# Optimization experiments

Hardware: AMD Instinct MI355X
Metric: run time of the kernel (lower is better)

Reference implementation:

```python
import jax, jax.numpy as jnp
import numpy as np

B, D, C = 4096, 768, 80
PRIV = np.arange(0, 20)        # privileged label indices
NONPRIV = np.arange(20, 80)    # non-privileged label indices
EPS = 1e-8
BETA = 1.0
EPSILON = 0.1
DIMS = [768, 256, 64, 16, 4, 1]


def setup_inputs() -> dict:
    key = jax.random.key(0)
    ks = jax.random.split(key, 12)
    inp = {
        "hidden": jax.random.normal(ks[0], (B, D), dtype=jnp.float32),
        "labels": jax.random.randint(ks[1], (B, C), 0, 2, dtype=jnp.int32),
    }
    ki = 2
    for wpref, bpref in (("W", "b"), ("rW", "rb")):
        for i in range(5):
            din, dout = DIMS[i], DIMS[i + 1]
            inp[f"{wpref}{i+1}"] = (jax.random.normal(ks[ki], (C, din, dout), dtype=jnp.float32)
                                     * (1.0 / np.sqrt(din)))
            inp[f"{bpref}{i+1}"] = jnp.zeros((C, dout), dtype=jnp.float32)
            ki += 1
    return inp


def _scores(hidden, Ws, bs):
    # c independent MLP heads applied to the same hidden state, batched over c.
    x = jnp.einsum('bd,cdh->bch', hidden, Ws[0]) + bs[0]  # (b, c, 256)
    for W, b in zip(Ws[1:], bs[1:]):
        x = jnp.einsum('bch,cho->bco', jax.nn.relu(x), W) + b
    return jax.nn.sigmoid(x[..., 0])  # (b, c)


def _bce(p, y):
    p = jnp.clip(p, EPS, 1.0 - EPS)
    return -(y * jnp.log(p) + (1.0 - y) * jnp.log1p(-p))


def _losses(scores, ref_scores, labels):
    ref_scores = jax.lax.stop_gradient(ref_scores)  # ref head is frozen
    # --- privileged pairwise margin loss (vectorized masked form) ---
    log_term = jnp.log(scores / (ref_scores + EPS) + EPS)  # (b, c)
    ps = scores[:, PRIV]                                   # (b, P)
    pos = labels[:, PRIV] == 1                             # (b, P)
    neg = labels == 0                                      # (b, c)
    # confusing negative k for positive privileged l: y_k==0 and s_k >= s_l
    conf = pos[:, :, None] & neg[:, None, :] & (scores[:, None, :] >= ps[:, :, None])
    h_w = log_term[:, PRIV][:, :, None] - log_term[:, None, :]   # (b, P, c)
    pair_loss = -jax.nn.log_sigmoid(BETA * h_w)
    n_pairs = conf.sum()
    total = jnp.where(conf, pair_loss, 0.0).sum()
    loss_priv = jnp.where(n_pairs > 0, total / jnp.maximum(n_pairs, 1), 0.0)
    # --- non-privileged hinged BCE ---
    y = labels[:, NONPRIV].astype(jnp.float32)
    loss_cur = _bce(scores[:, NONPRIV], y)
    loss_ref = jax.lax.stop_gradient(_bce(ref_scores[:, NONPRIV], y))
    loss_nonpriv = jnp.mean(jax.nn.relu(loss_cur - loss_ref - EPSILON))
    return jnp.stack([loss_priv, loss_nonpriv])


def reference(hidden, labels, W1, b1, W2, b2, W3, b3, W4, b4, W5, b5,
              rW1, rb1, rW2, rb2, rW3, rb3, rW4, rb4, rW5, rb5):
    scores = _scores(hidden, (W1, W2, W3, W4, W5), (b1, b2, b3, b4, b5))
    ref_scores = _scores(hidden, (rW1, rW2, rW3, rW4, rW5), (rb1, rb2, rb3, rb4, rb5))
    return _losses(scores, ref_scores, labels)
```

## Files before the change

kernel.cpp:

```cpp
#include <hip/hip_runtime.h>
#include <math.h>

typedef __attribute__((ext_vector_type(8))) short short8;
typedef __attribute__((ext_vector_type(4))) float f32x4;

#define Bn   4096
#define Dn   768
#define Cn   80
#define H1   256
#define H2   64
#define H3   16
#define H4   4

__device__ inline ushort f2bf(float f) {
    union { float f; unsigned u; } v; v.f = f;
    unsigned r = v.u + 0x7fffu + ((v.u >> 16) & 1u);
    return (ushort)(r >> 16);
}
__device__ inline unsigned pack2(float a, float b) {
    return (unsigned)f2bf(a) | ((unsigned)f2bf(b) << 16);
}
__device__ inline void load_lds16(const void* g, void* l) {
    __builtin_amdgcn_global_load_lds(
        (const __attribute__((address_space(1))) void*)g,
        (__attribute__((address_space(3))) void*)l, 16, 0, 0);
}

#define FENCE() asm volatile("" ::: "memory")
#define BAR() do { FENCE(); __builtin_amdgcn_sched_barrier(0); \
                   __builtin_amdgcn_s_barrier(); \
                   __builtin_amdgcn_sched_barrier(0); FENCE(); } while (0)
#define VMCNT4() do { asm volatile("s_waitcnt vmcnt(4)" ::: "memory"); \
                      __builtin_amdgcn_sched_barrier(0); } while (0)
#define VMCNT0() do { asm volatile("s_waitcnt vmcnt(0)" ::: "memory"); \
                      __builtin_amdgcn_sched_barrier(0); } while (0)

__global__ __launch_bounds__(256)
void convert_hidden(const float* __restrict__ hidden, ushort* __restrict__ hbs)
{
    const int t = threadIdx.x;
    const int kt = blockIdx.x;
    const int bt = blockIdx.y;
    char* out = (char*)(hbs + ((size_t)bt * 12 + kt) * 4096);
    #pragma unroll
    for (int ch = 0; ch < 2; ++ch) {
        const int o = (ch * 256 + t) * 16;
        const int row = o >> 7;
        const int slot = (o >> 4) & 7;
        const int ss = slot ^ (row & 7);
        const float* src = hidden + (size_t)(bt * 64 + row) * Dn + kt * 64 + ss * 8;
        const float4 f0 = ((const float4*)src)[0];
        const float4 f1 = ((const float4*)src)[1];
        uint4 w;
        w.x = pack2(f0.x, f0.y); w.y = pack2(f0.z, f0.w);
        w.z = pack2(f1.x, f1.y); w.w = pack2(f1.z, f1.w);
        *(uint4*)(out + o) = w;
    }
}

__global__ __launch_bounds__(256)
void convert_w1(const float* __restrict__ W, const float* __restrict__ rW,
                ushort* __restrict__ dst)
{
    __shared__ float l[32 * H1];
    const int t   = threadIdx.x;
    const int kt2 = blockIdx.x;
    const int c   = blockIdx.y;
    const int set = blockIdx.z;
    const float* src = (set ? rW : W) + ((size_t)c * Dn + kt2 * 32) * H1;
    #pragma unroll
    for (int i = 0; i < 8; ++i)
        ((float4*)l)[i * 256 + t] = ((const float4*)src)[i * 256 + t];
    __syncthreads();
    char* out = (char*)dst + (((size_t)set * Cn + c) * 24 + kt2) * 16384;
    #pragma unroll
    for (int rd = 0; rd < 4; ++rd) {
        const int o = (rd * 256 + t) * 16;
        const int n = o >> 6;
        const int s = (o >> 4) & 3;
        const int kk0 = (s ^ (n & 3)) * 8;
        uint4 w;
        w.x = pack2(l[(kk0 + 0) * H1 + n], l[(kk0 + 1) * H1 + n]);
        w.y = pack2(l[(kk0 + 2) * H1 + n], l[(kk0 + 3) * H1 + n]);
        w.z = pack2(l[(kk0 + 4) * H1 + n], l[(kk0 + 5) * H1 + n]);
        w.w = pack2(l[(kk0 + 6) * H1 + n], l[(kk0 + 7) * H1 + n]);
        *(uint4*)(out + o) = w;
    }
}

__global__ __launch_bounds__(256)
void convert_w23(const float* __restrict__ W2, const float* __restrict__ rW2,
                 const float* __restrict__ W3, const float* __restrict__ rW3,
                 ushort* __restrict__ dstW2, ushort* __restrict__ dstW3)
{
    __shared__ float l[64 * H2];
    const int t   = threadIdx.x;
    const int bx  = blockIdx.x;
    const int c   = blockIdx.y;
    const int set = blockIdx.z;

    if (bx < 4) {
        const float* src = (set ? rW2 : W2) + ((size_t)c * H1 + bx * 64) * H2;
        #pragma unroll
        for (int i = 0; i < 4; ++i)
            ((float4*)l)[i * 256 + t] = ((const float4*)src)[i * 256 + t];
        __syncthreads();
        char* out = (char*)dstW2 + (((size_t)set * Cn + c) * 4 + bx) * 8192;
        #pragma unroll
        for (int rd = 0; rd < 2; ++rd) {
            const int idx = rd * 256 + t;
            const int n = idx >> 3;
            const int s = idx & 7;
            const int o = n * 128 + ((s << 4) ^ ((n & 7) << 4));
            const int kk0 = s * 8;
            uint4 w;
            w.x = pack2(l[(kk0 + 0) * H2 + n], l[(kk0 + 1) * H2 + n]);
            w.y = pack2(l[(kk0 + 2) * H2 + n], l[(kk0 + 3) * H2 + n]);
            w.z = pack2(l[(kk0 + 4) * H2 + n], l[(kk0 + 5) * H2 + n]);
            w.w = pack2(l[(kk0 + 6) * H2 + n], l[(kk0 + 7) * H2 + n]);
            *(uint4*)(out + o) = w;
        }
    } else if (t < 128) {
        const float* src = (set ? rW3 : W3) + (size_t)c * (H2 * H3);
        char* out = (char*)dstW3 + ((size_t)set * Cn + c) * 2048;
        const int o = t * 16;
        const int n = o >> 7;
        const int slot = (o >> 4) & 7;
        const int kk0 = (slot ^ (n & 7)) * 8;
        uint4 w;
        w.x = pack2(src[(kk0 + 0) * H3 + n], src[(kk0 + 1) * H3 + n]);
        w.y = pack2(src[(kk0 + 2) * H3 + n], src[(kk0 + 3) * H3 + n]);
        w.z = pack2(src[(kk0 + 4) * H3 + n], src[(kk0 + 5) * H3 + n]);
        w.w = pack2(src[(kk0 + 6) * H3 + n], src[(kk0 + 7) * H3 + n]);
        *(uint4*)(out + o) = w;
    }
}


__device__ __forceinline__ void stage_a(char* lds, const char* hbs_b, int p, int h,
                                        int kt, int bt0, int t) {
    const char* g = hbs_b + ((size_t)((bt0 + h * 2) * 12 + kt)) * 8192 + t * 16;
    char* l = lds + p * 32768 + h * 16384 + t * 16;
    load_lds16(g,         l);
    load_lds16(g + 98304, l + 8192);
}
__device__ __forceinline__ void stage_b(char* lds, const char* w1b, int p, int kh,
                                        int kt, int t) {
    const char* g = w1b + ((size_t)(kt * 2 + kh)) * 16384 + t * 16;
    char* l = lds + 65536 + p * 32768 + kh * 16384 + t * 16;
    load_lds16(g,        l);
    load_lds16(g + 8192, l + 8192);
}

template<int KS, int MH>
__device__ __forceinline__ void phase_reads(const char* lds, int p, int wr, int wc,
                                            int lrow, int lk, short8 breg[4], short8 areg[4]) {
    if (MH == 0) {
        #pragma unroll
        for (int nt = 0; nt < 4; ++nt) {
            const int col = wc * 64 + nt * 16 + lrow;
            breg[nt] = *(const short8*)(lds + 65536 + p * 32768 + KS * 16384
                          + col * 64 + ((2 * lk) ^ ((col & 3) << 4)));
        }
    }
    #pragma unroll
    for (int m4 = 0; m4 < 4; ++m4) {
        const int mt = MH * 4 + m4;
        const int ir = (mt & 3) * 16 + lrow;
        const int koff = KS * 64 + lk * 2;
        areg[m4] = *(const short8*)(lds + p * 32768 + (wr * 2 + (mt >> 2)) * 8192
                      + ir * 128 + (koff ^ ((ir & 7) << 4)));
    }
}

template<int MH>
__device__ __forceinline__ void phase_mfma(const short8 breg[4], const short8 areg[4],
                                           f32x4 acc[8][4]) {
    __builtin_amdgcn_s_setprio(1);
    #pragma unroll
    for (int m4 = 0; m4 < 4; ++m4)
        #pragma unroll
        for (int nt = 0; nt < 4; ++nt)
            acc[MH * 4 + m4][nt] = __builtin_amdgcn_mfma_f32_16x16x32_bf16(
                breg[nt], areg[m4], acc[MH * 4 + m4][nt], 0, 0, 0);
    __builtin_amdgcn_s_setprio(0);
}

__global__ __launch_bounds__(512, 2)
void scores_mfma_256(const ushort* __restrict__ hbs, const ushort* __restrict__ W1ts,
                     const ushort* __restrict__ W2ts, const ushort* __restrict__ W3ts,
                     const float* __restrict__ b1, const float* __restrict__ rb1,
                     const float* __restrict__ b2, const float* __restrict__ rb2,
                     const float* __restrict__ b3, const float* __restrict__ rb3,
                     const float* __restrict__ W4, const float* __restrict__ rW4,
                     const float* __restrict__ b4, const float* __restrict__ rb4,
                     const float* __restrict__ W5, const float* __restrict__ rW5,
                     const float* __restrict__ b5, const float* __restrict__ rb5,
                     float* __restrict__ scores)
{
    __shared__ uint4 smv[131072 / 16];
    char* lds = (char*)smv;

    const int t = threadIdx.x;
    const int wid = t >> 6, lane = t & 63;
    const int lrow = lane & 15;
    const int lkg  = lane >> 4;
    const int lk   = lkg * 8;
    const int wr = wid >> 2, wc = wid & 3;

    const int cpx = 2560 >> 3;
    const int wg  = (blockIdx.x & 7) * cpx + (blockIdx.x >> 3);
    const int set = wg / 1280;
    const int rem = wg % 1280;
    const int c   = rem / 16;
    const int bt0 = (rem % 16) * 4;

    const float* pb1 = set ? rb1 : b1;
    const float* pb2 = set ? rb2 : b2;
    const float* pb3 = set ? rb3 : b3;
    const float* pW4 = set ? rW4 : W4;  const float* pb4 = set ? rb4 : b4;
    const float* pW5 = set ? rW5 : W5;  const float* pb5 = set ? rb5 : b5;

    const char* hbs_b = (const char*)hbs;
    const char* w1b   = (const char*)W1ts + (size_t)(set * Cn + c) * 393216;

    f32x4 acc[8][4];
    #pragma unroll
    for (int i = 0; i < 8; ++i)
        #pragma unroll
        for (int j = 0; j < 4; ++j)
            acc[i][j] = (f32x4){0.f, 0.f, 0.f, 0.f};

    stage_a(lds, hbs_b, 0, 0, 0, bt0, t);
    stage_a(lds, hbs_b, 0, 1, 0, bt0, t);
    stage_b(lds, w1b, 0, 0, 0, t);
    stage_b(lds, w1b, 0, 1, 0, t);
    stage_b(lds, w1b, 1, 0, 1, t);
    stage_b(lds, w1b, 1, 1, 1, t);
    VMCNT4();
    BAR();

    short8 breg[4], areg[4];
    for (int j = 0; j < 12; ++j) {
        const int p  = j & 1;
        const int ja = (j + 1) % 12;
        const int jb = (j + 2) % 12;
        phase_reads<0, 0>(lds, p, wr, wc, lrow, lk, breg, areg);
        stage_a(lds, hbs_b, p ^ 1, 0, ja, bt0, t);
        BAR(); phase_mfma<0>(breg, areg, acc); BAR();
        phase_reads<0, 1>(lds, p, wr, wc, lrow, lk, breg, areg);
        stage_a(lds, hbs_b, p ^ 1, 1, ja, bt0, t);
        BAR(); phase_mfma<1>(breg, areg, acc); BAR();
        phase_reads<1, 0>(lds, p, wr, wc, lrow, lk, breg, areg);
        stage_b(lds, w1b, p, 0, jb, t);
        BAR(); phase_mfma<0>(breg, areg, acc); BAR();
        phase_reads<1, 1>(lds, p, wr, wc, lrow, lk, breg, areg);
        stage_b(lds, w1b, p, 1, jb, t);
        VMCNT4();
        BAR(); phase_mfma<1>(breg, areg, acc); BAR();
    }
    VMCNT0();
    BAR();

    {
        float4 bias1[4];
        #pragma unroll
        for (int nt = 0; nt < 4; ++nt)
            bias1[nt] = *(const float4*)&pb1[(size_t)c * H1 + wc * 64 + nt * 16 + lkg * 4];
        #pragma unroll
        for (int mt = 0; mt < 8; ++mt) {
            const int row = wr * 128 + mt * 16 + lrow;
            const int swz = (row & 7) << 4;
            #pragma unroll
            for (int nt = 0; nt < 4; ++nt) {
                const float* bb = (const float*)&bias1[nt];
                uint2 w;
                w.x = pack2(fmaxf(acc[mt][nt][0] + bb[0], 0.f),
                            fmaxf(acc[mt][nt][1] + bb[1], 0.f));
                w.y = pack2(fmaxf(acc[mt][nt][2] + bb[2], 0.f),
                            fmaxf(acc[mt][nt][3] + bb[3], 0.f));
                const int off = row * 512 + ((wc * 128 + nt * 32 + lkg * 8) ^ swz);
                *(uint2*)(lds + off) = w;
            }
        }
    }
    BAR();

    f32x4 acc2[2][4];
    #pragma unroll
    for (int i = 0; i < 2; ++i)
        #pragma unroll
        for (int j = 0; j < 4; ++j)
            acc2[i][j] = (f32x4){0.f, 0.f, 0.f, 0.f};
    {
        const char* w2b = (const char*)W2ts + (size_t)(set * Cn + c) * 32768;
        #pragma unroll
        for (int ksz = 0; ksz < 8; ++ksz) {
            short8 b2r[4], a2[2];
            const int kk2 = (ksz & 1) * 32 + lk;
            #pragma unroll
            for (int nt = 0; nt < 4; ++nt) {
                const int col = nt * 16 + lrow;
                b2r[nt] = *(const short8*)(w2b + (ksz >> 1) * 8192
                             + ((col * 128 + 2 * kk2) ^ ((col & 7) << 4)));
            }
            const int k = ksz * 32 + lk;
            #pragma unroll
            for (int m2 = 0; m2 < 2; ++m2) {
                const int row = wid * 32 + m2 * 16 + lrow;
                a2[m2] = *(const short8*)(lds + ((row * 512 + 2 * k) ^ ((row & 7) << 4)));
            }
            #pragma unroll
            for (int m2 = 0; m2 < 2; ++m2)
                #pragma unroll
                for (int nt = 0; nt < 4; ++nt)
                    acc2[m2][nt] = __builtin_amdgcn_mfma_f32_16x16x32_bf16(
                        b2r[nt], a2[m2], acc2[m2][nt], 0, 0, 0);
        }
    }
    BAR();

    {
        float4 bias2[4];
        #pragma unroll
        for (int nt = 0; nt < 4; ++nt)
            bias2[nt] = *(const float4*)&pb2[(size_t)c * H2 + nt * 16 + lkg * 4];
        #pragma unroll
        for (int m2 = 0; m2 < 2; ++m2) {
            const int row = wid * 32 + m2 * 16 + lrow;
            const int swz = (row & 7) << 4;
            #pragma unroll
            for (int nt = 0; nt < 4; ++nt) {
                const float* bb = (const float*)&bias2[nt];
                uint2 w;
                w.x = pack2(fmaxf(acc2[m2][nt][0] + bb[0], 0.f),
                            fmaxf(acc2[m2][nt][1] + bb[1], 0.f));
                w.y = pack2(fmaxf(acc2[m2][nt][2] + bb[2], 0.f),
                            fmaxf(acc2[m2][nt][3] + bb[3], 0.f));
                const int off = row * 128 + ((nt * 32 + lkg * 8) ^ swz);
                *(uint2*)(lds + off) = w;
            }
        }
    }
    BAR();

    {
        const char* w3t = (const char*)W3ts + (size_t)(set * Cn + c) * 2048;
        short8 w3f[2];
        #pragma unroll
        for (int ks = 0; ks < 2; ++ks)
            w3f[ks] = *(const short8*)(w3t + lrow * 128
                         + ((2 * (ks * 32 + lk)) ^ ((lrow & 7) << 4)));
        f32x4 acc3[2];
        #pragma unroll
        for (int m2 = 0; m2 < 2; ++m2) acc3[m2] = (f32x4){0.f, 0.f, 0.f, 0.f};
        #pragma unroll
        for (int m2 = 0; m2 < 2; ++m2)
            #pragma unroll
            for (int ks = 0; ks < 2; ++ks) {
                const int row = wid * 32 + m2 * 16 + lrow;
                const short8 xf = *(const short8*)(lds + row * 128
                                     + ((2 * (ks * 32 + lk)) ^ ((row & 7) << 4)));
                acc3[m2] = __builtin_amdgcn_mfma_f32_16x16x32_bf16(
                    w3f[ks], xf, acc3[m2], 0, 0, 0);
            }

        const float4 b3v = *(const float4*)&pb3[(size_t)c * H3 + lkg * 4];
        const float* w4c = pW4 + (size_t)c * (H3 * H4);
        float4 w4r[4];
        #pragma unroll
        for (int r = 0; r < 4; ++r)
            w4r[r] = *(const float4*)&w4c[(lkg * 4 + r) * H4];
        const float4 b4v = *(const float4*)&pb4[(size_t)c * H4];
        const float4 w5v = *(const float4*)&pW5[(size_t)c * H4];
        const float bb5 = pb5[c];

        #pragma unroll
        for (int m2 = 0; m2 < 2; ++m2) {
            float p4[4] = {0.f, 0.f, 0.f, 0.f};
            #pragma unroll
            for (int r = 0; r < 4; ++r) {
                const float x3 = fmaxf(acc3[m2][r] + ((const float*)&b3v)[r], 0.f);
                const float* wr4 = (const float*)&w4r[r];
                #pragma unroll
                for (int o = 0; o < 4; ++o)
                    p4[o] = fmaf(x3, wr4[o], p4[o]);
            }
            #pragma unroll
            for (int o = 0; o < 4; ++o) {
                p4[o] += __shfl_xor(p4[o], 16, 64);
                p4[o] += __shfl_xor(p4[o], 32, 64);
            }
            float x5 = bb5;
            #pragma unroll
            for (int o = 0; o < 4; ++o)
                x5 = fmaf(fmaxf(p4[o] + ((const float*)&b4v)[o], 0.f),
                          ((const float*)&w5v)[o], x5);
            const float sc = 1.f / (1.f + expf(-x5));
            if (lkg == 0)
                scores[((size_t)set * Bn + bt0 * 64 + wid * 32 + m2 * 16 + lrow) * Cn + c] = sc;
        }
    }
}

__device__ inline float bce_f(float p, float y) {
    p = fminf(fmaxf(p, 1e-8f), 1.0f - 1e-8f);
    return -(y * logf(p) + (1.f - y) * log1pf(-p));
}

__global__ __launch_bounds__(128)
void loss_kernel(const float* __restrict__ scores, const int* __restrict__ labels,
                 float* __restrict__ pair_sum, float* __restrict__ np_sum,
                 int* __restrict__ pair_cnt)
{
    __shared__ float ss[Cn], lt[Cn];
    __shared__ int lab[Cn];
    __shared__ float redf[128], redn[128];
    __shared__ int redi[128];

    const int b = blockIdx.x, t = threadIdx.x;
    float np_local = 0.f, ps_local = 0.f;
    int pc_local = 0;

    if (t < Cn) {
        const float s  = scores[(size_t)b * Cn + t];
        const float sr = scores[(size_t)Bn * Cn + (size_t)b * Cn + t];
        const int l = labels[(size_t)b * Cn + t];
        ss[t] = s; lab[t] = l;
        lt[t] = logf(s / (sr + 1e-8f) + 1e-8f);
        if (t >= 20) {
            const float y = (float)l;
            np_local = fmaxf(bce_f(s, y) - bce_f(sr, y) - 0.1f, 0.f);
        }
    }
    __syncthreads();
    if (t < Cn && lab[t] == 0) {
        const float sj = ss[t], ltj = lt[t];
        #pragma unroll
        for (int i = 0; i < 20; ++i) {
            if (lab[i] == 1 && sj >= ss[i]) {
                const float z = -(lt[i] - ltj);
                ps_local += fmaxf(z, 0.f) + log1pf(expf(-fabsf(z)));
                pc_local++;
            }
        }
    }
    redf[t] = ps_local; redn[t] = np_local; redi[t] = pc_local;
    __syncthreads();
    for (int s = 64; s > 0; s >>= 1) {
        if (t < s) { redf[t] += redf[t + s]; redn[t] += redn[t + s]; redi[t] += redi[t + s]; }
        __syncthreads();
    }
    if (t == 0) { pair_sum[b] = redf[0]; np_sum[b] = redn[0]; pair_cnt[b] = redi[0]; }
}

__global__ __launch_bounds__(1024)
void final_kernel(const float* __restrict__ pair_sum, const int* __restrict__ pair_cnt,
                  const float* __restrict__ np_sum, float* __restrict__ out)
{
    __shared__ float r1[1024], r2[1024];
    __shared__ int ri[1024];
    const int t = threadIdx.x;
    float s1 = 0.f, s2 = 0.f; int c1 = 0;
    for (int i = t; i < Bn; i += 1024) { s1 += pair_sum[i]; c1 += pair_cnt[i]; s2 += np_sum[i]; }
    r1[t] = s1; r2[t] = s2; ri[t] = c1;
    __syncthreads();
    for (int s = 512; s > 0; s >>= 1) {
        if (t < s) { r1[t] += r1[t + s]; r2[t] += r2[t + s]; ri[t] += ri[t + s]; }
        __syncthreads();
    }
    if (t == 0) {
        const int n = ri[0];
        out[0] = (n > 0) ? (r1[0] / (float)(n > 1 ? n : 1)) : 0.f;
        out[1] = r2[0] / (float)(Bn * 60);
    }
}

static inline size_t alup(size_t x) { return (x + 4095) & ~(size_t)4095; }

extern "C" void kernel_launch(void* const* d_in, const int* in_sizes, int n_in,
                              void* d_out, int out_size, void* d_ws, size_t ws_size,
                              hipStream_t stream)
{
    const float* hidden = (const float*)d_in[0];
    const int*   labels = (const int*)d_in[1];
    const float* W1 = (const float*)d_in[2];   const float* b1 = (const float*)d_in[3];
    const float* W2 = (const float*)d_in[4];   const float* b2 = (const float*)d_in[5];
    const float* W3 = (const float*)d_in[6];   const float* b3 = (const float*)d_in[7];
    const float* W4 = (const float*)d_in[8];   const float* b4 = (const float*)d_in[9];
    const float* W5 = (const float*)d_in[10];  const float* b5 = (const float*)d_in[11];
    const float* rW1 = (const float*)d_in[12]; const float* rb1 = (const float*)d_in[13];
    const float* rW2 = (const float*)d_in[14]; const float* rb2 = (const float*)d_in[15];
    const float* rW3 = (const float*)d_in[16]; const float* rb3 = (const float*)d_in[17];
    const float* rW4 = (const float*)d_in[18]; const float* rb4 = (const float*)d_in[19];
    const float* rW5 = (const float*)d_in[20]; const float* rb5 = (const float*)d_in[21];

    char* ws = (char*)d_ws;
    const size_t off_scores = 0;
    const size_t sz_scores  = (size_t)2 * Bn * Cn * 4;
    const size_t off_pair   = alup(off_scores + sz_scores);
    const size_t sz_pair    = (size_t)3 * Bn * 4;
    const size_t off_hbs    = alup(off_pair + sz_pair);
    const size_t sz_hbs     = (size_t)Bn * Dn * 2;
    const size_t off_w1t    = alup(off_hbs + sz_hbs);
    const size_t sz_w1t     = (size_t)2 * Cn * 24 * 16384;
    const size_t off_w2t    = alup(off_w1t + sz_w1t);
    const size_t sz_w2t     = (size_t)2 * Cn * 4 * 8192;
    const size_t off_w3t    = alup(off_w2t + sz_w2t);

    float* scoresb  = (float*)(ws + off_scores);
    float* pair_sum = (float*)(ws + off_pair);
    float* np_sum   = pair_sum + Bn;
    int*   pair_cnt = (int*)(np_sum + Bn);
    float* out      = (float*)d_out;

    ushort* hbs  = (ushort*)(ws + off_hbs);
    ushort* W1ts = (ushort*)(ws + off_w1t);
    ushort* W2ts = (ushort*)(ws + off_w2t);
    ushort* W3ts = (ushort*)(ws + off_w3t);

    convert_hidden<<<dim3(12, Bn / 64), 256, 0, stream>>>(hidden, hbs);
    convert_w1<<<dim3(24, Cn, 2), 256, 0, stream>>>(W1, rW1, W1ts);
    convert_w23<<<dim3(5, Cn, 2), 256, 0, stream>>>(W2, rW2, W3, rW3, W2ts, W3ts);

    scores_mfma_256<<<2560, 512, 0, stream>>>(hbs, W1ts, W2ts, W3ts,
        b1, rb1, b2, rb2, b3, rb3, W4, rW4, b4, rb4, W5, rW5, b5, rb5,
        scoresb);
    loss_kernel<<<Bn, 128, 0, stream>>>(scoresb, labels, pair_sum, np_sum, pair_cnt);
    final_kernel<<<1, 1024, 0, stream>>>(pair_sum, pair_cnt, np_sum, out);
}
```

Before: 353.6 us.

## Shrink fused MLP tile to 128 rows with triple-buffered K=32 pipeline

Reworks the main scores kernel from 256-row tiles to 128-row tiles, doubling the grid and cutting LDS from 128KB to 72KB so four 512-thread blocks may fit per CU. The K loop changes from a double-buffered 64-wide step split into four phases to a triple-buffered 32-wide step with one MFMA burst per iteration. The hidden-state conversion layout and swizzle change to match. This raises occupancy and simplifies the pipeline, at the cost of loading each W1 slice twice as often (half the reuse per load) and more barriers per unit of work.

```diff
diff --git a/kernel.cpp b/kernel.cpp
--- a/kernel.cpp
+++ b/kernel.cpp
@@ -30,7 +30,7 @@
 #define BAR() do { FENCE(); __builtin_amdgcn_sched_barrier(0); \
                    __builtin_amdgcn_s_barrier(); \
                    __builtin_amdgcn_sched_barrier(0); FENCE(); } while (0)
-#define VMCNT4() do { asm volatile("s_waitcnt vmcnt(4)" ::: "memory"); \
+#define VMCNT3() do { asm volatile("s_waitcnt vmcnt(3)" ::: "memory"); \
                       __builtin_amdgcn_sched_barrier(0); } while (0)
 #define VMCNT0() do { asm volatile("s_waitcnt vmcnt(0)" ::: "memory"); \
                       __builtin_amdgcn_sched_barrier(0); } while (0)
@@ -41,14 +41,14 @@
     const int t = threadIdx.x;
     const int kt = blockIdx.x;
     const int bt = blockIdx.y;
-    char* out = (char*)(hbs + ((size_t)bt * 12 + kt) * 4096);
+    char* out = (char*)hbs + ((size_t)bt * 24 + kt) * 8192;
     #pragma unroll
     for (int ch = 0; ch < 2; ++ch) {
         const int o = (ch * 256 + t) * 16;
-        const int row = o >> 7;
-        const int slot = (o >> 4) & 7;
-        const int ss = slot ^ (row & 7);
-        const float* src = hidden + (size_t)(bt * 64 + row) * Dn + kt * 64 + ss * 8;
+        const int r = o >> 6;
+        const int s = (o >> 4) & 3;
+        const int k0 = (s ^ (r & 3)) * 8;
+        const float* src = hidden + (size_t)(bt * 128 + r) * Dn + kt * 32 + k0;
         const float4 f0 = ((const float4*)src)[0];
         const float4 f1 = ((const float4*)src)[1];
         uint4 w;
@@ -137,57 +137,18 @@
 }
 
 
-__device__ __forceinline__ void stage_a(char* lds, const char* hbs_b, int p, int h,
-                                        int kt, int bt0, int t) {
-    const char* g = hbs_b + ((size_t)((bt0 + h * 2) * 12 + kt)) * 8192 + t * 16;
-    char* l = lds + p * 32768 + h * 16384 + t * 16;
-    load_lds16(g,         l);
-    load_lds16(g + 98304, l + 8192);
-}
-__device__ __forceinline__ void stage_b(char* lds, const char* w1b, int p, int kh,
-                                        int kt, int t) {
-    const char* g = w1b + ((size_t)(kt * 2 + kh)) * 16384 + t * 16;
-    char* l = lds + 65536 + p * 32768 + kh * 16384 + t * 16;
+__device__ __forceinline__ void stageA(char* lds, const char* hb, int slot, int kt, int t) {
+    load_lds16(hb + (size_t)kt * 8192 + t * 16, lds + slot * 8192 + t * 16);
+}
+__device__ __forceinline__ void stageB(char* lds, const char* w1b, int slot, int kt, int t) {
+    const char* g = w1b + (size_t)kt * 16384 + t * 16;
+    char* l = lds + 24576 + slot * 16384 + t * 16;
     load_lds16(g,        l);
     load_lds16(g + 8192, l + 8192);
 }
 
-template<int KS, int MH>
-__device__ __forceinline__ void phase_reads(const char* lds, int p, int wr, int wc,
-                                            int lrow, int lk, short8 breg[4], short8 areg[4]) {
-    if (MH == 0) {
-        #pragma unroll
-        for (int nt = 0; nt < 4; ++nt) {
-            const int col = wc * 64 + nt * 16 + lrow;
-            breg[nt] = *(const short8*)(lds + 65536 + p * 32768 + KS * 16384
-                          + col * 64 + ((2 * lk) ^ ((col & 3) << 4)));
-        }
-    }
-    #pragma unroll
-    for (int m4 = 0; m4 < 4; ++m4) {
-        const int mt = MH * 4 + m4;
-        const int ir = (mt & 3) * 16 + lrow;
-        const int koff = KS * 64 + lk * 2;
-        areg[m4] = *(const short8*)(lds + p * 32768 + (wr * 2 + (mt >> 2)) * 8192
-                      + ir * 128 + (koff ^ ((ir & 7) << 4)));
-    }
-}
-
-template<int MH>
-__device__ __forceinline__ void phase_mfma(const short8 breg[4], const short8 areg[4],
-                                           f32x4 acc[8][4]) {
-    __builtin_amdgcn_s_setprio(1);
-    #pragma unroll
-    for (int m4 = 0; m4 < 4; ++m4)
-        #pragma unroll
-        for (int nt = 0; nt < 4; ++nt)
-            acc[MH * 4 + m4][nt] = __builtin_amdgcn_mfma_f32_16x16x32_bf16(
-                breg[nt], areg[m4], acc[MH * 4 + m4][nt], 0, 0, 0);
-    __builtin_amdgcn_s_setprio(0);
-}
-
-__global__ __launch_bounds__(512, 2)
-void scores_mfma_256(const ushort* __restrict__ hbs, const ushort* __restrict__ W1ts,
+__global__ __launch_bounds__(512, 4)
+void scores_mfma_128(const ushort* __restrict__ hbs, const ushort* __restrict__ W1ts,
                      const ushort* __restrict__ W2ts, const ushort* __restrict__ W3ts,
                      const float* __restrict__ b1, const float* __restrict__ rb1,
                      const float* __restrict__ b2, const float* __restrict__ rb2,
@@ -198,7 +159,7 @@
                      const float* __restrict__ b5, const float* __restrict__ rb5,
                      float* __restrict__ scores)
 {
-    __shared__ uint4 smv[131072 / 16];
+    __shared__ uint4 smv[73728 / 16];
     char* lds = (char*)smv;
 
     const int t = threadIdx.x;
@@ -208,12 +169,12 @@
     const int lk   = lkg * 8;
     const int wr = wid >> 2, wc = wid & 3;
 
-    const int cpx = 2560 >> 3;
+    const int cpx = 5120 >> 3;
     const int wg  = (blockIdx.x & 7) * cpx + (blockIdx.x >> 3);
-    const int set = wg / 1280;
-    const int rem = wg % 1280;
-    const int c   = rem / 16;
-    const int bt0 = (rem % 16) * 4;
+    const int set = wg / 2560;
+    const int rem = wg % 2560;
+    const int c   = rem / 32;
+    const int bt  = rem % 32;
 
     const float* pb1 = set ? rb1 : b1;
     const float* pb2 = set ? rb2 : b2;
@@ -221,43 +182,56 @@
     const float* pW4 = set ? rW4 : W4;  const float* pb4 = set ? rb4 : b4;
     const float* pW5 = set ? rW5 : W5;  const float* pb5 = set ? rb5 : b5;
 
-    const char* hbs_b = (const char*)hbs;
-    const char* w1b   = (const char*)W1ts + (size_t)(set * Cn + c) * 393216;
-
-    f32x4 acc[8][4];
+    const char* hb  = (const char*)hbs + (size_t)bt * 196608;
+    const char* w1b = (const char*)W1ts + (size_t)(set * Cn + c) * 393216;
+
+    f32x4 acc[4][4];
     #pragma unroll
-    for (int i = 0; i < 8; ++i)
+    for (int i = 0; i < 4; ++i)
         #pragma unroll
         for (int j = 0; j < 4; ++j)
             acc[i][j] = (f32x4){0.f, 0.f, 0.f, 0.f};
 
-    stage_a(lds, hbs_b, 0, 0, 0, bt0, t);
-    stage_a(lds, hbs_b, 0, 1, 0, bt0, t);
-    stage_b(lds, w1b, 0, 0, 0, t);
-    stage_b(lds, w1b, 0, 1, 0, t);
-    stage_b(lds, w1b, 1, 0, 1, t);
-    stage_b(lds, w1b, 1, 1, 1, t);
-    VMCNT4();
+    stageA(lds, hb, 0, 0, t);  stageB(lds, w1b, 0, 0, t);
+    stageA(lds, hb, 1, 1, t);  stageB(lds, w1b, 1, 1, t);
+    VMCNT3();
     BAR();
 
-    short8 breg[4], areg[4];
-    for (int j = 0; j < 12; ++j) {
-        const int p  = j & 1;
-        const int ja = (j + 1) % 12;
-        const int jb = (j + 2) % 12;
-        phase_reads<0, 0>(lds, p, wr, wc, lrow, lk, breg, areg);
-        stage_a(lds, hbs_b, p ^ 1, 0, ja, bt0, t);
-        BAR(); phase_mfma<0>(breg, areg, acc); BAR();
-        phase_reads<0, 1>(lds, p, wr, wc, lrow, lk, breg, areg);
-        stage_a(lds, hbs_b, p ^ 1, 1, ja, bt0, t);
-        BAR(); phase_mfma<1>(breg, areg, acc); BAR();
-        phase_reads<1, 0>(lds, p, wr, wc, lrow, lk, breg, areg);
-        stage_b(lds, w1b, p, 0, jb, t);
-        BAR(); phase_mfma<0>(breg, areg, acc); BAR();
-        phase_reads<1, 1>(lds, p, wr, wc, lrow, lk, breg, areg);
-        stage_b(lds, w1b, p, 1, jb, t);
-        VMCNT4();
-        BAR(); phase_mfma<1>(breg, areg, acc); BAR();
+    #pragma unroll 3
+    for (int j = 0; j < 24; ++j) {
+        const int rs = j % 3;
+        short8 breg[4], areg[4];
+        {
+            const char* bb = lds + 24576 + rs * 16384;
+            const char* ab = lds + rs * 8192;
+            #pragma unroll
+            for (int nt = 0; nt < 4; ++nt) {
+                const int col = wc * 64 + nt * 16 + lrow;
+                breg[nt] = *(const short8*)(bb + col * 64 + ((2 * lk) ^ ((col & 3) << 4)));
+            }
+            #pragma unroll
+            for (int mt = 0; mt < 4; ++mt) {
+                const int row = wr * 64 + mt * 16 + lrow;
+                areg[mt] = *(const short8*)(ab + row * 64 + ((2 * lk) ^ ((row & 3) << 4)));
+            }
+        }
+        {
+            const int ws = (j + 2) % 3;
+            int ka = j + 2; if (ka >= 24) ka -= 24;
+            stageA(lds, hb, ws, ka, t);
+            stageB(lds, w1b, ws, ka, t);
+        }
+        VMCNT3();
+        BAR();
+        __builtin_amdgcn_s_setprio(1);
+        #pragma unroll
+        for (int mt = 0; mt < 4; ++mt)
+            #pragma unroll
+            for (int nt = 0; nt < 4; ++nt)
+                acc[mt][nt] = __builtin_amdgcn_mfma_f32_16x16x32_bf16(
+                    breg[nt], areg[mt], acc[mt][nt], 0, 0, 0);
+        __builtin_amdgcn_s_setprio(0);
+        BAR();
     }
     VMCNT0();
     BAR();
@@ -268,8 +242,8 @@
         for (int nt = 0; nt < 4; ++nt)
             bias1[nt] = *(const float4*)&pb1[(size_t)c * H1 + wc * 64 + nt * 16 + lkg * 4];
         #pragma unroll
-        for (int mt = 0; mt < 8; ++mt) {
-            const int row = wr * 128 + mt * 16 + lrow;
+        for (int mt = 0; mt < 4; ++mt) {
+            const int row = wr * 64 + mt * 16 + lrow;
             const int swz = (row & 7) << 4;
             #pragma unroll
             for (int nt = 0; nt < 4; ++nt) {
@@ -286,17 +260,16 @@
     }
     BAR();
 
-    f32x4 acc2[2][4];
+    f32x4 acc2[4];
     #pragma unroll
-    for (int i = 0; i < 2; ++i)
-        #pragma unroll
-        for (int j = 0; j < 4; ++j)
-            acc2[i][j] = (f32x4){0.f, 0.f, 0.f, 0.f};
+    for (int j = 0; j < 4; ++j) acc2[j] = (f32x4){0.f, 0.f, 0.f, 0.f};
     {
         const char* w2b = (const char*)W2ts + (size_t)(set * Cn + c) * 32768;
+        const int row = wid * 16 + lrow;
+        const int swzr = (row & 7) << 4;
         #pragma unroll
         for (int ksz = 0; ksz < 8; ++ksz) {
-            short8 b2r[4], a2[2];
+            short8 b2r[4];
             const int kk2 = (ksz & 1) * 32 + lk;
             #pragma unroll
             for (int nt = 0; nt < 4; ++nt) {
@@ -305,41 +278,29 @@
                              + ((col * 128 + 2 * kk2) ^ ((col & 7) << 4)));
             }
             const int k = ksz * 32 + lk;
-            #pragma unroll
-            for (int m2 = 0; m2 < 2; ++m2) {
-                const int row = wid * 32 + m2 * 16 + lrow;
-                a2[m2] = *(const short8*)(lds + ((row * 512 + 2 * k) ^ ((row & 7) << 4)));
-            }
-            #pragma unroll
-            for (int m2 = 0; m2 < 2; ++m2)
-                #pragma unroll
-                for (int nt = 0; nt < 4; ++nt)
-                    acc2[m2][nt] = __builtin_amdgcn_mfma_f32_16x16x32_bf16(
-                        b2r[nt], a2[m2], acc2[m2][nt], 0, 0, 0);
+            const short8 a2 = *(const short8*)(lds + ((row * 512 + 2 * k) ^ swzr));
+            #pragma unroll
+            for (int nt = 0; nt < 4; ++nt)
+                acc2[nt] = __builtin_amdgcn_mfma_f32_16x16x32_bf16(
+                    b2r[nt], a2, acc2[nt], 0, 0, 0);
         }
     }
     BAR();
 
     {
-        float4 bias2[4];
-        #pragma unroll
-        for (int nt = 0; nt < 4; ++nt)
-            bias2[nt] = *(const float4*)&pb2[(size_t)c * H2 + nt * 16 + lkg * 4];
-        #pragma unroll
-        for (int m2 = 0; m2 < 2; ++m2) {
-            const int row = wid * 32 + m2 * 16 + lrow;
-            const int swz = (row & 7) << 4;
-            #pragma unroll
-            for (int nt = 0; nt < 4; ++nt) {
-                const float* bb = (const float*)&bias2[nt];
-                uint2 w;
-                w.x = pack2(fmaxf(acc2[m2][nt][0] + bb[0], 0.f),
-                            fmaxf(acc2[m2][nt][1] + bb[1], 0.f));
-                w.y = pack2(fmaxf(acc2[m2][nt][2] + bb[2], 0.f),
-                            fmaxf(acc2[m2][nt][3] + bb[3], 0.f));
-                const int off = row * 128 + ((nt * 32 + lkg * 8) ^ swz);
-                *(uint2*)(lds + off) = w;
-            }
+        const int row = wid * 16 + lrow;
+        const int swz = (row & 7) << 4;
+        #pragma unroll
+        for (int nt = 0; nt < 4; ++nt) {
+            const float4 bv = *(const float4*)&pb2[(size_t)c * H2 + nt * 16 + lkg * 4];
+            const float* bb = (const float*)&bv;
+            uint2 w;
+            w.x = pack2(fmaxf(acc2[nt][0] + bb[0], 0.f),
+                        fmaxf(acc2[nt][1] + bb[1], 0.f));
+            w.y = pack2(fmaxf(acc2[nt][2] + bb[2], 0.f),
+                        fmaxf(acc2[nt][3] + bb[3], 0.f));
+            const int off = row * 128 + ((nt * 32 + lkg * 8) ^ swz);
+            *(uint2*)(lds + off) = w;
         }
     }
     BAR();
@@ -351,19 +312,14 @@
         for (int ks = 0; ks < 2; ++ks)
             w3f[ks] = *(const short8*)(w3t + lrow * 128
                          + ((2 * (ks * 32 + lk)) ^ ((lrow & 7) << 4)));
-        f32x4 acc3[2];
-        #pragma unroll
-        for (int m2 = 0; m2 < 2; ++m2) acc3[m2] = (f32x4){0.f, 0.f, 0.f, 0.f};
-        #pragma unroll
-        for (int m2 = 0; m2 < 2; ++m2)
-            #pragma unroll
-            for (int ks = 0; ks < 2; ++ks) {
-                const int row = wid * 32 + m2 * 16 + lrow;
-                const short8 xf = *(const short8*)(lds + row * 128
-                                     + ((2 * (ks * 32 + lk)) ^ ((row & 7) << 4)));
-                acc3[m2] = __builtin_amdgcn_mfma_f32_16x16x32_bf16(
-                    w3f[ks], xf, acc3[m2], 0, 0, 0);
-            }
+        f32x4 acc3 = (f32x4){0.f, 0.f, 0.f, 0.f};
+        const int row = wid * 16 + lrow;
+        #pragma unroll
+        for (int ks = 0; ks < 2; ++ks) {
+            const short8 xf = *(const short8*)(lds + row * 128
+                                 + ((2 * (ks * 32 + lk)) ^ ((row & 7) << 4)));
+            acc3 = __builtin_amdgcn_mfma_f32_16x16x32_bf16(w3f[ks], xf, acc3, 0, 0, 0);
+        }
 
         const float4 b3v = *(const float4*)&pb3[(size_t)c * H3 + lkg * 4];
         const float* w4c = pW4 + (size_t)c * (H3 * H4);
@@ -375,31 +331,28 @@
         const float4 w5v = *(const float4*)&pW5[(size_t)c * H4];
         const float bb5 = pb5[c];
 
-        #pragma unroll
-        for (int m2 = 0; m2 < 2; ++m2) {
-            float p4[4] = {0.f, 0.f, 0.f, 0.f};
-            #pragma unroll
-            for (int r = 0; r < 4; ++r) {
-                const float x3 = fmaxf(acc3[m2][r] + ((const float*)&b3v)[r], 0.f);
-                const float* wr4 = (const float*)&w4r[r];
-                #pragma unroll
-                for (int o = 0; o < 4; ++o)
-                    p4[o] = fmaf(x3, wr4[o], p4[o]);
-            }
-            #pragma unroll
-            for (int o = 0; o < 4; ++o) {
-                p4[o] += __shfl_xor(p4[o], 16, 64);
-                p4[o] += __shfl_xor(p4[o], 32, 64);
-            }
-            float x5 = bb5;
+        float p4[4] = {0.f, 0.f, 0.f, 0.f};
+        #pragma unroll
+        for (int r = 0; r < 4; ++r) {
+            const float x3 = fmaxf(acc3[r] + ((const float*)&b3v)[r], 0.f);
+            const float* wr4 = (const float*)&w4r[r];
             #pragma unroll
             for (int o = 0; o < 4; ++o)
-                x5 = fmaf(fmaxf(p4[o] + ((const float*)&b4v)[o], 0.f),
-                          ((const float*)&w5v)[o], x5);
-            const float sc = 1.f / (1.f + expf(-x5));
-            if (lkg == 0)
-                scores[((size_t)set * Bn + bt0 * 64 + wid * 32 + m2 * 16 + lrow) * Cn + c] = sc;
-        }
+                p4[o] = fmaf(x3, wr4[o], p4[o]);
+        }
+        #pragma unroll
+        for (int o = 0; o < 4; ++o) {
+            p4[o] += __shfl_xor(p4[o], 16, 64);
+            p4[o] += __shfl_xor(p4[o], 32, 64);
+        }
+        float x5 = bb5;
+        #pragma unroll
+        for (int o = 0; o < 4; ++o)
+            x5 = fmaf(fmaxf(p4[o] + ((const float*)&b4v)[o], 0.f),
+                      ((const float*)&w5v)[o], x5);
+        const float sc = 1.f / (1.f + expf(-x5));
+        if (lkg == 0)
+            scores[((size_t)set * Bn + bt * 128 + wid * 16 + lrow) * Cn + c] = sc;
     }
 }
 
@@ -519,11 +472,11 @@
     ushort* W2ts = (ushort*)(ws + off_w2t);
     ushort* W3ts = (ushort*)(ws + off_w3t);
 
-    convert_hidden<<<dim3(12, Bn / 64), 256, 0, stream>>>(hidden, hbs);
+    convert_hidden<<<dim3(24, Bn / 128), 256, 0, stream>>>(hidden, hbs);
     convert_w1<<<dim3(24, Cn, 2), 256, 0, stream>>>(W1, rW1, W1ts);
     convert_w23<<<dim3(5, Cn, 2), 256, 0, stream>>>(W2, rW2, W3, rW3, W2ts, W3ts);
 
-    scores_mfma_256<<<2560, 512, 0, stream>>>(hbs, W1ts, W2ts, W3ts,
+    scores_mfma_128<<<5120, 512, 0, stream>>>(hbs, W1ts, W2ts, W3ts,
         b1, rb1, b2, rb2, b3, rb3, W4, rW4, b4, rb4, W5, rW5, b5, rb5,
         scoresb);
     loss_kernel<<<Bn, 128, 0, stream>>>(scoresb, labels, pair_sum, np_sum, pair_cnt);
```

New measurement: 378.4 us. +7.0%, slower.
